# Kernel optimization log

Hardware: AMD Instinct MI355X
Metric: run time of the kernel (lower is better)

The kernel has to match this reference:

```python
import jax, jax.numpy as jnp
import numpy as np

PAD = 2
EPS = 1e-5


def setup_inputs() -> dict:
    key = jax.random.key(0)
    k1, = jax.random.split(key, 1)
    N, C, H, W = 32, 64, 224, 224
    x = jax.random.normal(k1, (N, C, H, W), dtype=jnp.float32)
    bn_weight = jnp.ones((C,), dtype=jnp.float32)
    bn_bias = jnp.zeros((C,), dtype=jnp.float32)
    post_scale = jnp.asarray(0.5, dtype=jnp.float32)
    return {"x": x, "bn_weight": bn_weight, "bn_bias": bn_bias, "post_scale": post_scale}


def reference(x, bn_weight, bn_bias, post_scale):
    # 1) reflection pad H and W by PAD on each side -> (N, C, H+2p, W+2p)
    pad_x = jnp.pad(x, ((0, 0), (0, 0), (PAD, PAD), (PAD, PAD)), mode="reflect")
    # 2-4) GLU over [pad_x, roll(pad_x)] along channels == pad_x * sigmoid(roll)
    pad_x_roll = jnp.roll(pad_x, shift=1, axis=1)
    gated = pad_x * jax.nn.sigmoid(pad_x_roll)
    # 5) global average pool -> (N, C)
    pooled = gated.mean(axis=(2, 3))
    # 6) BatchNorm1d (training mode: batch stats, biased variance, affine)
    mu = pooled.mean(axis=0)
    var = pooled.var(axis=0)  # biased, matches BN normalization
    normed = (pooled - mu) / jnp.sqrt(var + EPS) * bn_weight + bn_bias
    # 7-9) sigmoid reweight + channel-mean residual + scalar scale + exact GELU
    scale = jax.nn.sigmoid(normed)[:, :, None, None]
    channel_mean = pad_x.mean(axis=(2, 3), keepdims=True)
    out = jax.nn.gelu((gated * scale + channel_mean) * post_scale, approximate=False)
    return out.reshape(out.shape[0], -1)
```

## Files before the change

### kernel.cpp

```cpp
#include <hip/hip_runtime.h>
#include <math.h>

#define NB 32
#define CB 64
#define HH 224
#define WW 224
#define PADP 2
#define HP (HH + 2*PADP)
#define WP (WW + 2*PADP)
#define HW (HH*WW)
#define HWP (HP*WP)
#define EPSV 1e-5f
#define CHUNKS 49

typedef float v4f __attribute__((ext_vector_type(4)));

__device__ __forceinline__ float fsig(float v) {
    float e = __expf(-v);
    return __builtin_amdgcn_rcpf(1.0f + e);
}
__device__ __forceinline__ float fgelu(float v) {
    float t = v * (1.5957691216f + 0.0713548162f * v * v);
    return v * fsig(t);
}
__device__ __forceinline__ float edgew(int w) {
    return 1.0f + (float)((w == 1) | (w == 2) | (w == WW-3) | (w == WW-2));
}

__global__ __launch_bounds__(256) void k_pool3(const float* __restrict__ x,
                                               float* __restrict__ partG,
                                               float* __restrict__ partX) {
    int b = blockIdx.x;
    int n = b / CHUNKS;
    int chunk = b - n * CHUNKS;
    int wave = threadIdx.x >> 6;
    int lane = threadIdx.x & 63;

    int p0 = chunk * 1024 + lane * 4;
    float4 wgt[4];
    #pragma unroll
    for (int m = 0; m < 4; ++m) {
        int pm = p0 + m * 256;
        int h  = pm / WW;
        int w0 = pm - h * WW;
        float wh = 1.0f + (float)((h == 1) | (h == 2) | (h == HH-3) | (h == HH-2));
        wgt[m].x = wh * edgew(w0);
        wgt[m].y = wh * edgew(w0 + 1);
        wgt[m].z = wh * edgew(w0 + 2);
        wgt[m].w = wh * edgew(w0 + 3);
    }

    const float* xn = x + (size_t)n * CB * HW;
    int c0 = wave * 16;
    int cg = (c0 + CB - 1) & (CB - 1);
    float4 prev[4];
    #pragma unroll
    for (int m = 0; m < 4; ++m)
        prev[m] = *(const float4*)(xn + (size_t)cg * HW + p0 + m * 256);

    for (int k = 0; k < 16; ++k) {
        int c = c0 + k;
        float4 cur[4];
        #pragma unroll
        for (int m = 0; m < 4; ++m)
            cur[m] = *(const float4*)(xn + (size_t)c * HW + p0 + m * 256);
        float sG = 0.f, sX = 0.f;
        #pragma unroll
        for (int m = 0; m < 4; ++m) {
            sG += wgt[m].x * cur[m].x * fsig(prev[m].x);
            sG += wgt[m].y * cur[m].y * fsig(prev[m].y);
            sG += wgt[m].z * cur[m].z * fsig(prev[m].z);
            sG += wgt[m].w * cur[m].w * fsig(prev[m].w);
            sX += wgt[m].x * cur[m].x + wgt[m].y * cur[m].y
                + wgt[m].z * cur[m].z + wgt[m].w * cur[m].w;
            prev[m] = cur[m];
        }
        #pragma unroll
        for (int off = 32; off >= 1; off >>= 1) {
            sG += __shfl_xor(sG, off);
            sX += __shfl_xor(sX, off);
        }
        if (lane == 0) {
            size_t idx = ((size_t)n * CB + c) * CHUNKS + chunk;
            partG[idx] = sG;
            partX[idx] = sX;
        }
    }
}

__global__ __launch_bounds__(256) void k_stats(const float* __restrict__ partG,
                                               const float* __restrict__ partX,
                                               const float* __restrict__ bnw,
                                               const float* __restrict__ bnb,
                                               float* __restrict__ cmean,
                                               float* __restrict__ scale) {
    int c = blockIdx.x;
    int t = threadIdx.x;
    int n = t >> 3, j0 = t & 7;
    float g = 0.f, xx = 0.f;
    for (int j = j0; j < CHUNKS; j += 8) {
        size_t idx = ((size_t)n * CB + c) * CHUNKS + j;
        g  += partG[idx];
        xx += partX[idx];
    }
    #pragma unroll
    for (int off = 4; off >= 1; off >>= 1) {
        g  += __shfl_xor(g, off);
        xx += __shfl_xor(xx, off);
    }
    __shared__ float lG[NB];
    if (j0 == 0) {
        lG[n] = g;
        cmean[n * CB + c] = xx * (1.0f / (float)HWP);
    }
    __syncthreads();
    if (t < NB) {
        float p = lG[t] * (1.0f / (float)HWP);
        float s = p;
        #pragma unroll
        for (int off = 16; off >= 1; off >>= 1) s += __shfl_xor(s, off);
        float mu = s * (1.0f / 32.0f);
        float d = p - mu;
        float q = d * d;
        #pragma unroll
        for (int off = 16; off >= 1; off >>= 1) q += __shfl_xor(q, off);
        float var = q * (1.0f / 32.0f);
        float normed = d * rsqrtf(var + EPSV) * bnw[c] + bnb[c];
        scale[t * CB + c] = 1.0f / (1.0f + expf(-normed));
    }
}

__global__ __launch_bounds__(256) void k_out(const float* __restrict__ x,
                                             const float* __restrict__ scale,
                                             const float* __restrict__ cmean,
                                             const float* __restrict__ post_scale,
                                             float* __restrict__ out) {
    int o = blockIdx.x;
    int w = (o & 7) * (NB * HP / 8) + (o >> 3);
    int n  = w / HP;
    int hp = w - n * HP;
    int rh = hp - PADP; rh = rh < 0 ? -rh : (rh >= HH ? 2*HH - 2 - rh : rh);
    int wave = threadIdx.x >> 6;
    int lane = threadIdx.x & 63;
    bool act = lane < 56;
    float ps = post_scale[0];

    const float* xrow = x + (size_t)n * CB * HW + (size_t)rh * WW;
    const float* sc_row = scale + n * CB;
    const float* cm_row = cmean + n * CB;

    int c0 = wave * 16;
    int cg = (c0 + CB - 1) & (CB - 1);
    v4f prev = {0.f, 0.f, 0.f, 0.f};
    if (act) prev = __builtin_nontemporal_load((const v4f*)(xrow + (size_t)cg * HW + 4 * lane));

    #pragma unroll
    for (int k = 0; k < 16; ++k) {
        int c = c0 + k;
        v4f cur = {0.f, 0.f, 0.f, 0.f};
        if (act) cur = __builtin_nontemporal_load((const v4f*)(xrow + (size_t)c * HW + 4 * lane));
        float scp = sc_row[c] * ps;
        float cmp = cm_row[c] * ps;
        float o0 = fgelu(fmaf(cur.x * fsig(prev.x), scp, cmp));
        float o1 = fgelu(fmaf(cur.y * fsig(prev.y), scp, cmp));
        float o2 = fgelu(fmaf(cur.z * fsig(prev.z), scp, cmp));
        float o3 = fgelu(fmaf(cur.w * fsig(prev.w), scp, cmp));
        float o1s = __shfl(o1, lane - 1);
        float o2s = __shfl(o2, lane - 1);
        float o3s = __shfl(o3, lane - 1);
        v4f st = { o2s, o3s, o0, o1 };
        if (lane == 0)  st = (v4f){ o2, o1, o0, o1 };
        if (lane == 56) st = (v4f){ o2s, o3s, o2s, o1s };
        if (lane < 57) {
            float* orow = out + ((size_t)n * CB + c) * HWP + (size_t)hp * WP;
            __builtin_nontemporal_store(st, (v4f*)(orow + 4 * lane));
        }
        prev = cur;
    }
}

extern "C" void kernel_launch(void* const* d_in, const int* in_sizes, int n_in,
                              void* d_out, int out_size, void* d_ws, size_t ws_size,
                              hipStream_t stream) {
    const float* x   = (const float*)d_in[0];
    const float* bnw = (const float*)d_in[1];
    const float* bnb = (const float*)d_in[2];
    const float* ps  = (const float*)d_in[3];
    float* out = (float*)d_out;

    size_t npart = (size_t)NB * CB * CHUNKS;
    float* partG  = (float*)d_ws;
    float* partX  = partG + npart;
    float* cmean  = partX + npart;
    float* scale  = cmean + NB * CB;

    k_pool3<<<NB * CHUNKS, 256, 0, stream>>>(x, partG, partX);
    k_stats<<<CB, 256, 0, stream>>>(partG, partX, bnw, bnb, cmean, scale);
    k_out<<<NB * HP, 256, 0, stream>>>(x, scale, cmean, ps, out);
}
```

Baseline: 252.8 us.

## Materialize gated activations in fp16 during pooling and reuse them in output pass

The pooling kernel now also writes the gated product x*sigmoid(roll(x)) to a half-precision workspace buffer. The output kernel then reads that buffer instead of re-reading two fp32 channels of x and recomputing the sigmoid. This removes the second fp32 read of x and one sigmoid per element in the output pass. The cost is an extra fp16 write and read of the whole tensor, so total memory traffic stays about the same. It also adds fp16 rounding of the gated values and needs a large workspace, with a fallback to the old path when the workspace is too small.

```diff
diff --git a/kernel.cpp b/kernel.cpp
--- a/kernel.cpp
+++ b/kernel.cpp
@@ -13,7 +13,8 @@
 #define EPSV 1e-5f
 #define CHUNKS 49
 
-typedef float v4f __attribute__((ext_vector_type(4)));
+typedef float   v4f __attribute__((ext_vector_type(4)));
+typedef _Float16 h4 __attribute__((ext_vector_type(4)));
 
 __device__ __forceinline__ float fsig(float v) {
     float e = __expf(-v);
@@ -27,7 +28,8 @@
     return 1.0f + (float)((w == 1) | (w == 2) | (w == WW-3) | (w == WW-2));
 }
 
-__global__ __launch_bounds__(256) void k_pool3(const float* __restrict__ x,
+__global__ __launch_bounds__(256) void k_pool5(const float* __restrict__ x,
+                                               _Float16* __restrict__ gat,
                                                float* __restrict__ partG,
                                                float* __restrict__ partX) {
     int b = blockIdx.x;
@@ -50,6 +52,70 @@
         wgt[m].w = wh * edgew(w0 + 3);
     }
 
+    const float* xn = x + (size_t)n * CB * HW;
+    _Float16* gn = gat + (size_t)n * CB * HW;
+    int c0 = wave * 16;
+    int cg = (c0 + CB - 1) & (CB - 1);
+    v4f prev[4];
+    #pragma unroll
+    for (int m = 0; m < 4; ++m)
+        prev[m] = __builtin_nontemporal_load((const v4f*)(xn + (size_t)cg * HW + p0 + m * 256));
+
+    for (int k = 0; k < 16; ++k) {
+        int c = c0 + k;
+        v4f cur[4];
+        #pragma unroll
+        for (int m = 0; m < 4; ++m)
+            cur[m] = __builtin_nontemporal_load((const v4f*)(xn + (size_t)c * HW + p0 + m * 256));
+        float sG = 0.f, sX = 0.f;
+        #pragma unroll
+        for (int m = 0; m < 4; ++m) {
+            float g0 = cur[m].x * fsig(prev[m].x);
+            float g1 = cur[m].y * fsig(prev[m].y);
+            float g2 = cur[m].z * fsig(prev[m].z);
+            float g3 = cur[m].w * fsig(prev[m].w);
+            sG += wgt[m].x * g0 + wgt[m].y * g1 + wgt[m].z * g2 + wgt[m].w * g3;
+            sX += wgt[m].x * cur[m].x + wgt[m].y * cur[m].y
+                + wgt[m].z * cur[m].z + wgt[m].w * cur[m].w;
+            *(h4*)(gn + (size_t)c * HW + p0 + m * 256) =
+                (h4){(_Float16)g0, (_Float16)g1, (_Float16)g2, (_Float16)g3};
+            prev[m] = cur[m];
+        }
+        #pragma unroll
+        for (int off = 32; off >= 1; off >>= 1) {
+            sG += __shfl_xor(sG, off);
+            sX += __shfl_xor(sX, off);
+        }
+        if (lane == 0) {
+            size_t idx = ((size_t)n * CB + c) * CHUNKS + chunk;
+            partG[idx] = sG;
+            partX[idx] = sX;
+        }
+    }
+}
+
+__global__ __launch_bounds__(256) void k_pool3(const float* __restrict__ x,
+                                               float* __restrict__ partG,
+                                               float* __restrict__ partX) {
+    int b = blockIdx.x;
+    int n = b / CHUNKS;
+    int chunk = b - n * CHUNKS;
+    int wave = threadIdx.x >> 6;
+    int lane = threadIdx.x & 63;
+
+    int p0 = chunk * 1024 + lane * 4;
+    float4 wgt[4];
+    #pragma unroll
+    for (int m = 0; m < 4; ++m) {
+        int pm = p0 + m * 256;
+        int h  = pm / WW;
+        int w0 = pm - h * WW;
+        float wh = 1.0f + (float)((h == 1) | (h == 2) | (h == HH-3) | (h == HH-2));
+        wgt[m].x = wh * edgew(w0);
+        wgt[m].y = wh * edgew(w0 + 1);
+        wgt[m].z = wh * edgew(w0 + 2);
+        wgt[m].w = wh * edgew(w0 + 3);
+    }
     const float* xn = x + (size_t)n * CB * HW;
     int c0 = wave * 16;
     int cg = (c0 + CB - 1) & (CB - 1);
@@ -130,6 +196,50 @@
     }
 }
 
+__global__ __launch_bounds__(256) void k_outg(const _Float16* __restrict__ gat,
+                                              const float* __restrict__ scale,
+                                              const float* __restrict__ cmean,
+                                              const float* __restrict__ post_scale,
+                                              float* __restrict__ out) {
+    int o = blockIdx.x;
+    int w = (o & 7) * (NB * HP / 8) + (o >> 3);
+    int n  = w / HP;
+    int hp = w - n * HP;
+    int rh = hp - PADP; rh = rh < 0 ? -rh : (rh >= HH ? 2*HH - 2 - rh : rh);
+    int wave = threadIdx.x >> 6;
+    int lane = threadIdx.x & 63;
+    bool act = lane < 56;
+    float ps = post_scale[0];
+
+    const _Float16* grow = gat + (size_t)n * CB * HW + (size_t)rh * WW;
+    const float* sc_row = scale + n * CB;
+    const float* cm_row = cmean + n * CB;
+    int c0 = wave * 16;
+
+    #pragma unroll
+    for (int k = 0; k < 16; ++k) {
+        int c = c0 + k;
+        h4 g = (h4){(_Float16)0, (_Float16)0, (_Float16)0, (_Float16)0};
+        if (act) g = *(const h4*)(grow + (size_t)c * HW + 4 * lane);
+        float scp = sc_row[c] * ps;
+        float cmp = cm_row[c] * ps;
+        float o0 = fgelu(fmaf((float)g.x, scp, cmp));
+        float o1 = fgelu(fmaf((float)g.y, scp, cmp));
+        float o2 = fgelu(fmaf((float)g.z, scp, cmp));
+        float o3 = fgelu(fmaf((float)g.w, scp, cmp));
+        float o1s = __shfl(o1, lane - 1);
+        float o2s = __shfl(o2, lane - 1);
+        float o3s = __shfl(o3, lane - 1);
+        v4f st = { o2s, o3s, o0, o1 };
+        if (lane == 0)  st = (v4f){ o2, o1, o0, o1 };
+        if (lane == 56) st = (v4f){ o2s, o3s, o2s, o1s };
+        if (lane < 57) {
+            float* orow = out + ((size_t)n * CB + c) * HWP + (size_t)hp * WP;
+            __builtin_nontemporal_store(st, (v4f*)(orow + 4 * lane));
+        }
+    }
+}
+
 __global__ __launch_bounds__(256) void k_out(const float* __restrict__ x,
                                              const float* __restrict__ scale,
                                              const float* __restrict__ cmean,
@@ -148,7 +258,6 @@
     const float* xrow = x + (size_t)n * CB * HW + (size_t)rh * WW;
     const float* sc_row = scale + n * CB;
     const float* cm_row = cmean + n * CB;
-
     int c0 = wave * 16;
     int cg = (c0 + CB - 1) & (CB - 1);
     v4f prev = {0.f, 0.f, 0.f, 0.f};
@@ -189,12 +298,25 @@
     float* out = (float*)d_out;
 
     size_t npart = (size_t)NB * CB * CHUNKS;
-    float* partG  = (float*)d_ws;
-    float* partX  = partG + npart;
-    float* cmean  = partX + npart;
-    float* scale  = cmean + NB * CB;
-
-    k_pool3<<<NB * CHUNKS, 256, 0, stream>>>(x, partG, partX);
-    k_stats<<<CB, 256, 0, stream>>>(partG, partX, bnw, bnb, cmean, scale);
-    k_out<<<NB * HP, 256, 0, stream>>>(x, scale, cmean, ps, out);
-}
+    size_t ngat  = (size_t)NB * CB * HW;
+    size_t need  = ngat * 2 + (2 * npart + 2 * (size_t)NB * CB) * 4;
+
+    if (ws_size >= need) {
+        _Float16* gat  = (_Float16*)d_ws;
+        float* partG  = (float*)((char*)d_ws + ngat * 2);
+        float* partX  = partG + npart;
+        float* cmean  = partX + npart;
+        float* scale  = cmean + NB * CB;
+        k_pool5<<<NB * CHUNKS, 256, 0, stream>>>(x, gat, partG, partX);
+        k_stats<<<CB, 256, 0, stream>>>(partG, partX, bnw, bnb, cmean, scale);
+        k_outg<<<NB * HP, 256, 0, stream>>>(gat, scale, cmean, ps, out);
+    } else {
+        float* partG  = (float*)d_ws;
+        float* partX  = partG + npart;
+        float* cmean  = partX + npart;
+        float* scale  = cmean + NB * CB;
+        k_pool3<<<NB * CHUNKS, 256, 0, stream>>>(x, partG, partX);
+        k_stats<<<CB, 256, 0, stream>>>(partG, partX, bnw, bnb, cmean, scale);
+        k_out<<<NB * HP, 256, 0, stream>>>(x, scale, cmean, ps, out);
+    }
+}
```

New measurement: 242.0 us. 4.3% less time.
